# Kernel optimization log

Hardware: AMD Instinct MI355X
Metric: run time of the kernel (lower is better)

## Reference

```python
import jax, jax.numpy as jnp
import numpy as np

D_MODEL = 1024
NUM_HEADS = 16
THETA = 10000.0
NEG = -1000000.0  # masked_fill value used by the torch code


def _rope(x, token_positions, theta):
    # x: [B, H, S, d_head]; token_positions: [S] int
    d_k = x.shape[-1]
    half = d_k // 2
    j = jnp.arange(half, dtype=jnp.float32)
    inv_freq = theta ** (-(2.0 * j) / d_k)                      # [half]
    ang = token_positions.astype(jnp.float32)[:, None] * inv_freq  # [S, half]
    cos = jnp.cos(ang)
    sin = jnp.sin(ang)
    xp = x.reshape(x.shape[:-1] + (half, 2))  # adjacent pairs (pc, 2)
    x0, x1 = xp[..., 0], xp[..., 1]
    o0 = x0 * cos - x1 * sin
    o1 = x0 * sin + x1 * cos
    out = jnp.stack([o0, o1], axis=-1)
    return out.reshape(x.shape)


def setup_inputs() -> dict:
    key = jax.random.key(0)
    k0, k1, k2 = jax.random.split(key, 3)
    B, S, D = 2, 2048, D_MODEL
    std = (2.0 / (D + D)) ** 0.5
    X = jax.random.normal(k0, (B, S, D), dtype=jnp.float32)
    QKV_weights = jax.random.normal(k1, (3 * D, D), dtype=jnp.float32) * std
    O_weights = jax.random.normal(k2, (D, D), dtype=jnp.float32) * std
    token_positions = jnp.arange(S, dtype=jnp.int32)
    return {"X": X, "token_positions": token_positions,
            "QKV_weights": QKV_weights, "O_weights": O_weights}


def reference(X, token_positions, QKV_weights, O_weights):
    B, S, D = X.shape
    H = NUM_HEADS
    dh = D // H
    qkv = jnp.einsum('od,bsd->bso', QKV_weights, X)  # [B, S, 3D]
    Q, K, V = jnp.split(qkv, 3, axis=-1)

    def split_heads(t):
        return t.reshape(B, S, H, dh).transpose(0, 2, 1, 3)  # [B,H,S,dh]

    Q, K, V = split_heads(Q), split_heads(K), split_heads(V)
    Q = _rope(Q, token_positions, THETA)
    K = _rope(K, token_positions, THETA)

    scores = (jnp.einsum('bhqd,bhkd->bhqk', Q, K) / jnp.sqrt(jnp.float32(dh))).astype(jnp.float32)
    causal = jnp.tril(jnp.ones((S, S), dtype=bool))
    scores = jnp.where(causal, scores, NEG)
    probs = jax.nn.softmax(scores, axis=-1)
    attn = jnp.einsum('bhqk,bhkd->bhqd', probs, V.astype(jnp.float32)).astype(Q.dtype)
    attn = attn.transpose(0, 2, 1, 3).reshape(B, S, D)
    return jnp.einsum('od,bsd->bso', O_weights, attn)
```

## Files before the change

kernel.cpp:

```cpp
#include <hip/hip_runtime.h>
#include <math.h>

#define S_LEN 2048

using bf16x8  = __attribute__((ext_vector_type(8))) short;
using shortx4 = __attribute__((ext_vector_type(4))) short;
using f32x4   = __attribute__((ext_vector_type(4))) float;

static __device__ __forceinline__ short f2bf(float f) {
  unsigned u = __float_as_uint(f);
  u += 0x7fffu + ((u >> 16) & 1u);
  return (short)(u >> 16);
}
static __device__ __forceinline__ float bf2f(short s) {
  return __uint_as_float(((unsigned)(unsigned short)s) << 16);
}

#define GLD_LDS16(gptr, lptr)                                                  \
  __builtin_amdgcn_global_load_lds(                                            \
      (__attribute__((address_space(1))) void*)(gptr),                         \
      (__attribute__((address_space(3))) void*)(lptr), 16, 0, 0)

#define EXP2_SHIFT 20.0f

static __device__ __forceinline__ f32x4 exp2s4(f32x4 a) {
  return (f32x4){__builtin_amdgcn_exp2f(a[0] - EXP2_SHIFT),
                 __builtin_amdgcn_exp2f(a[1] - EXP2_SHIFT),
                 __builtin_amdgcn_exp2f(a[2] - EXP2_SHIFT),
                 __builtin_amdgcn_exp2f(a[3] - EXP2_SHIFT)};
}

__global__ __launch_bounds__(256) void init_kernel(const float* __restrict__ X,
                                                   const float* __restrict__ W1,
                                                   const float* __restrict__ W2,
                                                   const int* __restrict__ tok,
                                                   short* __restrict__ Xb,
                                                   short* __restrict__ W1b,
                                                   short* __restrict__ W2b,
                                                   float2* __restrict__ table) {
  if (blockIdx.x < 4096) {
    size_t idx = (size_t)(blockIdx.x * 256 + threadIdx.x) * 8;
    const float* src;
    short* dst;
    size_t off;
    if (idx < 4194304) { src = X; dst = Xb; off = idx; }
    else if (idx < 4194304 + 3145728) { src = W1; dst = W1b; off = idx - 4194304; }
    else { src = W2; dst = W2b; off = idx - (4194304 + 3145728); }
    float4 a = *(const float4*)(src + off);
    float4 b = *(const float4*)(src + off + 4);
    bf16x8 o = {f2bf(a.x), f2bf(a.y), f2bf(a.z), f2bf(a.w),
                f2bf(b.x), f2bf(b.y), f2bf(b.z), f2bf(b.w)};
    *(bf16x8*)(dst + off) = o;
  } else {
    int i = (blockIdx.x - 4096) * 256 + threadIdx.x;
    int s = i >> 5, j = i & 31;
    double pos = (double)tok[s];
    double ang = pos * pow(10000.0, -(double)j / 32.0);
    table[i] = make_float2((float)cos(ang), (float)sin(ang));
  }
}

template <int BM, typename OutT>
__global__ __launch_bounds__(256) void gemm_ll(const short* __restrict__ A,
                                               const short* __restrict__ B,
                                               OutT* __restrict__ C,
                                               int M, int N, int K) {
  constexpr int MI = BM / 32;
  constexpr int AI = BM / 64;
  __shared__ short As[BM * 32];
  __shared__ short Bs[128 * 32];
  const int tid  = threadIdx.x;
  const int lane = tid & 63;
  const int wv   = tid >> 6;
  const int wm   = (wv >> 1) * (BM / 2);
  const int wn   = (wv & 1) * 64;
  const int m16  = lane & 15;
  const int q4   = lane >> 4;
  const int rowBase = blockIdx.y * BM;
  const int colBase = blockIdx.x * 128;
  const int lrow = lane >> 2;
  const int lseg = lane & 3;

  f32x4 acc[MI][4];
#pragma unroll
  for (int i = 0; i < MI; ++i)
#pragma unroll
    for (int j = 0; j < 4; ++j) acc[i][j] = (f32x4){0.f, 0.f, 0.f, 0.f};

  const short* Agl = A + (size_t)rowBase * K;
  const short* Bgl = B + (size_t)colBase * K;

  for (int kk = 0; kk < K; kk += 32) {
#pragma unroll
    for (int i = 0; i < AI; ++i) {
      const int r0 = (wv * AI + i) * 16;
      GLD_LDS16(Agl + (size_t)(r0 + lrow) * K + kk + lseg * 8, &As[r0 * 32]);
    }
#pragma unroll
    for (int i = 0; i < 2; ++i) {
      const int r0 = (wv * 2 + i) * 16;
      GLD_LDS16(Bgl + (size_t)(r0 + lrow) * K + kk + lseg * 8, &Bs[r0 * 32]);
    }
    __syncthreads();

    bf16x8 af[MI], bfv[4];
#pragma unroll
    for (int mi = 0; mi < MI; ++mi)
      af[mi] = *(const bf16x8*)&As[(wm + mi * 16 + m16) * 32 + q4 * 8];
#pragma unroll
    for (int ni = 0; ni < 4; ++ni)
      bfv[ni] = *(const bf16x8*)&Bs[(wn + ni * 16 + m16) * 32 + q4 * 8];
#pragma unroll
    for (int mi = 0; mi < MI; ++mi)
#pragma unroll
      for (int ni = 0; ni < 4; ++ni)
        acc[mi][ni] = __builtin_amdgcn_mfma_f32_16x16x32_bf16(af[mi], bfv[ni], acc[mi][ni], 0, 0, 0);
    __syncthreads();
  }

#pragma unroll
  for (int mi = 0; mi < MI; ++mi)
#pragma unroll
    for (int ni = 0; ni < 4; ++ni) {
      const int rbase = rowBase + wm + mi * 16 + q4 * 4;
      const int cidx  = colBase + wn + ni * 16 + m16;
#pragma unroll
      for (int r = 0; r < 4; ++r) {
        float v = acc[mi][ni][r];
        if constexpr (sizeof(OutT) == 2)
          C[(size_t)(rbase + r) * N + cidx] = (OutT)f2bf(v);
        else
          C[(size_t)(rbase + r) * N + cidx] = (OutT)v;
      }
    }
}

__global__ __launch_bounds__(256) void prep_kernel(const short* __restrict__ qkvb,
                                                   const float2* __restrict__ table,
                                                   short* __restrict__ Qb,
                                                   short* __restrict__ Kb,
                                                   short* __restrict__ VT) {
  __shared__ __align__(16) short VtL[64 * 72];
  const int tid = threadIdx.x;
  const int st  = blockIdx.x, bh = blockIdx.y;
  const int b   = bh >> 4, h = bh & 15;
  const int r   = tid >> 2, seg = tid & 3;
  const int s   = st * 64 + r;
  const int pr  = (r & 15) * 4 + (r >> 4);
  const short* base = qkvb + (size_t)(b * S_LEN + s) * 3072 + h * 64 + seg * 16;
  const float QSCALE = 0.125f * 1.44269504f;

#pragma unroll
  for (int which = 0; which < 2; ++which) {
    const short* src = base + which * 1024;
    short in[16], ob[16];
    *(bf16x8*)&in[0] = ((const bf16x8*)src)[0];
    *(bf16x8*)&in[8] = ((const bf16x8*)src)[1];
#pragma unroll
    for (int p = 0; p < 8; ++p) {
      float x0 = bf2f(in[2 * p]), x1 = bf2f(in[2 * p + 1]);
      float2 cs = table[s * 32 + seg * 8 + p];
      float o0 = x0 * cs.x - x1 * cs.y;
      float o1 = x0 * cs.y + x1 * cs.x;
      if (which == 0) { o0 *= QSCALE; o1 *= QSCALE; }
      ob[2 * p]     = f2bf(o0);
      ob[2 * p + 1] = f2bf(o1);
    }
    short* dst = (which ? Kb : Qb) + ((size_t)bh * S_LEN + s) * 64 + seg * 16;
    ((bf16x8*)dst)[0] = *(bf16x8*)&ob[0];
    ((bf16x8*)dst)[1] = *(bf16x8*)&ob[8];
  }

  {
    const short* vsrc = base + 2048;
    short in[16];
    *(bf16x8*)&in[0] = ((const bf16x8*)vsrc)[0];
    *(bf16x8*)&in[8] = ((const bf16x8*)vsrc)[1];
#pragma unroll
    for (int d = 0; d < 16; ++d)
      VtL[(seg * 16 + d) * 72 + pr] = in[d];
  }
  __syncthreads();
  short* vdst = VT + ((size_t)bh * 64 + r) * S_LEN + st * 64 + seg * 16;
  ((bf16x8*)vdst)[0] = *(bf16x8*)&VtL[r * 72 + seg * 16];
  ((bf16x8*)vdst)[1] = *(bf16x8*)&VtL[r * 72 + seg * 16 + 8];
}

__global__ __launch_bounds__(256, 2) void attn_mfma(const short* __restrict__ Qb,
                                                    const short* __restrict__ Kb,
                                                    const short* __restrict__ VT,
                                                    short* __restrict__ attnb) {
  __shared__ __align__(16) short Ks[64 * 72];
  __shared__ __align__(16) short Vs[64 * 72];
  __shared__ __align__(16) short Ps[128 * 72];
  const int tid  = threadIdx.x;
  const int lane = tid & 63;
  const int w    = tid >> 6;
  const int m16  = lane & 15;
  const int quad = lane >> 4;
  const int bh   = blockIdx.x;
  const int jt   = 15 - blockIdx.y;
  const int b    = bh >> 4, h = bh & 15;
  const short* Qh = Qb + (size_t)bh * S_LEN * 64;
  const short* Kh = Kb + (size_t)bh * S_LEN * 64;
  const short* Vh = VT + (size_t)bh * 64 * S_LEN;

  const int srow = tid >> 3;
  const int seg  = tid & 7;

  const bf16x8 ones = {16256, 16256, 16256, 16256, 16256, 16256, 16256, 16256};

  const int q0 = jt * 128;
  const int ktiles = 2 * jt + 2;

  bf16x8 qf[2][2];
#pragma unroll
  for (int m = 0; m < 2; ++m)
#pragma unroll
    for (int ks = 0; ks < 2; ++ks)
      qf[m][ks] = *(const bf16x8*)(Qh + (size_t)(q0 + w * 32 + m * 16 + m16) * 64 + ks * 32 + quad * 8);

  f32x4 O[2][4], Lacc[2];
#pragma unroll
  for (int m = 0; m < 2; ++m) {
    Lacc[m] = (f32x4){0.f, 0.f, 0.f, 0.f};
#pragma unroll
    for (int c = 0; c < 4; ++c) O[m][c] = (f32x4){0.f, 0.f, 0.f, 0.f};
  }

  bf16x8 kst[2], vst[2];
#pragma unroll
  for (int i = 0; i < 2; ++i) {
    kst[i] = *(const bf16x8*)(Kh + (size_t)(i * 32 + srow) * 64 + seg * 8);
    vst[i] = *(const bf16x8*)(Vh + (size_t)(i * 32 + srow) * S_LEN + seg * 8);
  }

  for (int t = 0; t < ktiles; ++t) {
    {
#pragma unroll
      for (int i = 0; i < 2; ++i) {
        *(bf16x8*)&Ks[(i * 32 + srow) * 72 + seg * 8] = kst[i];
        *(bf16x8*)&Vs[(i * 32 + srow) * 72 + seg * 8] = vst[i];
      }
    }
    __syncthreads();

    if (t + 1 < ktiles) {
#pragma unroll
      for (int i = 0; i < 2; ++i) {
        kst[i] = *(const bf16x8*)(Kh + (size_t)((t + 1) * 64 + i * 32 + srow) * 64 + seg * 8);
        vst[i] = *(const bf16x8*)(Vh + (size_t)(i * 32 + srow) * S_LEN + (t + 1) * 64 + seg * 8);
      }
    }

    f32x4 sc[2][4];
#pragma unroll
    for (int m = 0; m < 2; ++m)
#pragma unroll
      for (int c = 0; c < 4; ++c) sc[m][c] = (f32x4){0.f, 0.f, 0.f, 0.f};
#pragma unroll
    for (int ks = 0; ks < 2; ++ks) {
#pragma unroll
      for (int c = 0; c < 4; ++c) {
        bf16x8 kf = *(const bf16x8*)&Ks[(c * 16 + m16) * 72 + ks * 32 + quad * 8];
#pragma unroll
        for (int m = 0; m < 2; ++m)
          sc[m][c] = __builtin_amdgcn_mfma_f32_16x16x32_bf16(qf[m][ks], kf, sc[m][c], 0, 0, 0);
      }
    }

    if (t >= ktiles - 2) {
#pragma unroll
      for (int m = 0; m < 2; ++m)
#pragma unroll
        for (int c = 0; c < 4; ++c) {
          const int kg = t * 64 + c * 16 + m16;
#pragma unroll
          for (int rr = 0; rr < 4; ++rr) {
            const int qg = q0 + w * 32 + m * 16 + quad * 4 + rr;
            if (kg > qg) sc[m][c][rr] = -1e30f;
          }
        }
    }

#pragma unroll
    for (int m = 0; m < 2; ++m) {
#pragma unroll
      for (int c = 0; c < 4; ++c) sc[m][c] = exp2s4(sc[m][c]);
#pragma unroll
      for (int rr = 0; rr < 4; ++rr) {
        shortx4 pk = {f2bf(sc[m][0][rr]), f2bf(sc[m][1][rr]),
                      f2bf(sc[m][2][rr]), f2bf(sc[m][3][rr])};
        *(shortx4*)&Ps[(w * 32 + m * 16 + quad * 4 + rr) * 72 + m16 * 4] = pk;
      }
    }
    __syncthreads();

#pragma unroll
    for (int ks = 0; ks < 2; ++ks) {
      bf16x8 pa[2];
#pragma unroll
      for (int m = 0; m < 2; ++m)
        pa[m] = *(const bf16x8*)&Ps[(w * 32 + m * 16 + m16) * 72 + ks * 32 + quad * 8];
#pragma unroll
      for (int c = 0; c < 4; ++c) {
        bf16x8 vb = *(const bf16x8*)&Vs[(c * 16 + m16) * 72 + ks * 32 + quad * 8];
#pragma unroll
        for (int m = 0; m < 2; ++m)
          O[m][c] = __builtin_amdgcn_mfma_f32_16x16x32_bf16(pa[m], vb, O[m][c], 0, 0, 0);
      }
#pragma unroll
      for (int m = 0; m < 2; ++m)
        Lacc[m] = __builtin_amdgcn_mfma_f32_16x16x32_bf16(pa[m], ones, Lacc[m], 0, 0, 0);
    }
    __syncthreads();
  }

#pragma unroll
  for (int m = 0; m < 2; ++m) {
    float inv[4];
#pragma unroll
    for (int rr = 0; rr < 4; ++rr) inv[rr] = __frcp_rn(Lacc[m][rr]);
#pragma unroll
    for (int c = 0; c < 4; ++c) {
      const int col = h * 64 + c * 16 + m16;
#pragma unroll
      for (int rr = 0; rr < 4; ++rr) {
        const int q = q0 + w * 32 + m * 16 + quad * 4 + rr;
        attnb[(size_t)(b * S_LEN + q) * 1024 + col] = f2bf(O[m][c][rr] * inv[rr]);
      }
    }
  }
}

extern "C" void kernel_launch(void* const* d_in, const int* in_sizes, int n_in,
                              void* d_out, int out_size, void* d_ws, size_t ws_size,
                              hipStream_t stream) {
  const float* X    = (const float*)d_in[0];
  const int*   tok  = (const int*)d_in[1];
  const float* Wqkv = (const float*)d_in[2];
  const float* Wo   = (const float*)d_in[3];
  float* out = (float*)d_out;

  char* w = (char*)d_ws;
  float2* table = (float2*)w;
  short*  qkvb  = (short*)(w + 524288);
  short*  Qb    = (short*)(w + 524288 + 25165824);
  short*  Kb    = Qb + 4194304;
  short*  VTt   = Kb + 4194304;
  short*  Xb    = VTt + 4194304;
  short*  Wqkvb = Xb + 4194304;
  short*  Wob   = Wqkvb + 3145728;
  short*  attnb = qkvb;

  hipLaunchKernelGGL(init_kernel, dim3(4352), dim3(256), 0, stream,
                     X, Wqkv, Wo, tok, Xb, Wqkvb, Wob, table);
  hipLaunchKernelGGL((gemm_ll<128, short>), dim3(24, 32), dim3(256), 0, stream,
                     Xb, Wqkvb, qkvb, 4096, 3072, 1024);
  hipLaunchKernelGGL(prep_kernel, dim3(32, 32), dim3(256), 0, stream,
                     qkvb, table, Qb, Kb, VTt);
  hipLaunchKernelGGL(attn_mfma, dim3(32, 16), dim3(256), 0, stream,
                     Qb, Kb, VTt, attnb);
  hipLaunchKernelGGL((gemm_ll<64, float>), dim3(8, 64), dim3(256), 0, stream,
                     attnb, Wob, out, 4096, 1024, 1024);
}
```

Measured before the change: 193.9 us.

## Compute transposed S^T so P stays in registers, dropping LDS round trip

```diff
diff --git a/kernel.cpp b/kernel.cpp
--- a/kernel.cpp
+++ b/kernel.cpp
@@ -28,6 +28,10 @@
                  __builtin_amdgcn_exp2f(a[1] - EXP2_SHIFT),
                  __builtin_amdgcn_exp2f(a[2] - EXP2_SHIFT),
                  __builtin_amdgcn_exp2f(a[3] - EXP2_SHIFT)};
+}
+
+static __device__ __forceinline__ int sigma64(int k) {
+  return (k & 0x20) | ((k & 0x0C) << 1) | ((k & 0x10) >> 2) | (k & 3);
 }
 
 __global__ __launch_bounds__(256) void init_kernel(const float* __restrict__ X,
@@ -146,7 +150,7 @@
   const int b   = bh >> 4, h = bh & 15;
   const int r   = tid >> 2, seg = tid & 3;
   const int s   = st * 64 + r;
-  const int pr  = (r & 15) * 4 + (r >> 4);
+  const int pr  = sigma64(r);
   const short* base = qkvb + (size_t)(b * S_LEN + s) * 3072 + h * 64 + seg * 16;
   const float QSCALE = 0.125f * 1.44269504f;
 
@@ -190,16 +194,17 @@
                                                     const short* __restrict__ Kb,
                                                     const short* __restrict__ VT,
                                                     short* __restrict__ attnb) {
-  __shared__ __align__(16) short Ks[64 * 72];
-  __shared__ __align__(16) short Vs[64 * 72];
-  __shared__ __align__(16) short Ps[128 * 72];
+  __shared__ __align__(16) short Smem[9216];
+  short* Ks = Smem;
+  short* Vs = Smem + 64 * 72;
   const int tid  = threadIdx.x;
   const int lane = tid & 63;
   const int w    = tid >> 6;
   const int m16  = lane & 15;
-  const int quad = lane >> 4;
+  const int q4   = lane >> 4;
   const int bh   = blockIdx.x;
-  const int jt   = 15 - blockIdx.y;
+  const int jtx  = blockIdx.y;
+  const int jt   = (jtx < 8) ? (15 - jtx) : (jtx - 8);
   const int b    = bh >> 4, h = bh & 15;
   const short* Qh = Qb + (size_t)bh * S_LEN * 64;
   const short* Kh = Kb + (size_t)bh * S_LEN * 64;
@@ -215,17 +220,17 @@
 
   bf16x8 qf[2][2];
 #pragma unroll
-  for (int m = 0; m < 2; ++m)
+  for (int n = 0; n < 2; ++n)
 #pragma unroll
     for (int ks = 0; ks < 2; ++ks)
-      qf[m][ks] = *(const bf16x8*)(Qh + (size_t)(q0 + w * 32 + m * 16 + m16) * 64 + ks * 32 + quad * 8);
+      qf[n][ks] = *(const bf16x8*)(Qh + (size_t)(q0 + w * 32 + n * 16 + m16) * 64 + ks * 32 + q4 * 8);
 
   f32x4 O[2][4], Lacc[2];
 #pragma unroll
-  for (int m = 0; m < 2; ++m) {
-    Lacc[m] = (f32x4){0.f, 0.f, 0.f, 0.f};
-#pragma unroll
-    for (int c = 0; c < 4; ++c) O[m][c] = (f32x4){0.f, 0.f, 0.f, 0.f};
+  for (int n = 0; n < 2; ++n) {
+    Lacc[n] = (f32x4){0.f, 0.f, 0.f, 0.f};
+#pragma unroll
+    for (int c = 0; c < 4; ++c) O[n][c] = (f32x4){0.f, 0.f, 0.f, 0.f};
   }
 
   bf16x8 kst[2], vst[2];
@@ -236,12 +241,10 @@
   }
 
   for (int t = 0; t < ktiles; ++t) {
-    {
-#pragma unroll
-      for (int i = 0; i < 2; ++i) {
-        *(bf16x8*)&Ks[(i * 32 + srow) * 72 + seg * 8] = kst[i];
-        *(bf16x8*)&Vs[(i * 32 + srow) * 72 + seg * 8] = vst[i];
-      }
+#pragma unroll
+    for (int i = 0; i < 2; ++i) {
+      *(bf16x8*)&Ks[(i * 32 + srow) * 72 + seg * 8] = kst[i];
+      *(bf16x8*)&Vs[(i * 32 + srow) * 72 + seg * 8] = vst[i];
     }
     __syncthreads();
 
@@ -255,81 +258,80 @@
 
     f32x4 sc[2][4];
 #pragma unroll
-    for (int m = 0; m < 2; ++m)
-#pragma unroll
-      for (int c = 0; c < 4; ++c) sc[m][c] = (f32x4){0.f, 0.f, 0.f, 0.f};
+    for (int n = 0; n < 2; ++n)
+#pragma unroll
+      for (int c = 0; c < 4; ++c) sc[n][c] = (f32x4){0.f, 0.f, 0.f, 0.f};
 #pragma unroll
     for (int ks = 0; ks < 2; ++ks) {
 #pragma unroll
       for (int c = 0; c < 4; ++c) {
-        bf16x8 kf = *(const bf16x8*)&Ks[(c * 16 + m16) * 72 + ks * 32 + quad * 8];
-#pragma unroll
-        for (int m = 0; m < 2; ++m)
-          sc[m][c] = __builtin_amdgcn_mfma_f32_16x16x32_bf16(qf[m][ks], kf, sc[m][c], 0, 0, 0);
+        bf16x8 kf = *(const bf16x8*)&Ks[(c * 16 + m16) * 72 + ks * 32 + q4 * 8];
+#pragma unroll
+        for (int n = 0; n < 2; ++n)
+          sc[n][c] = __builtin_amdgcn_mfma_f32_16x16x32_bf16(kf, qf[n][ks], sc[n][c], 0, 0, 0);
       }
     }
 
     if (t >= ktiles - 2) {
 #pragma unroll
-      for (int m = 0; m < 2; ++m)
+      for (int n = 0; n < 2; ++n)
 #pragma unroll
         for (int c = 0; c < 4; ++c) {
-          const int kg = t * 64 + c * 16 + m16;
+          const int qg = q0 + w * 32 + n * 16 + m16;
 #pragma unroll
           for (int rr = 0; rr < 4; ++rr) {
-            const int qg = q0 + w * 32 + m * 16 + quad * 4 + rr;
-            if (kg > qg) sc[m][c][rr] = -1e30f;
+            const int kg = t * 64 + c * 16 + q4 * 4 + rr;
+            if (kg > qg) sc[n][c][rr] = -1e30f;
           }
         }
     }
 
-#pragma unroll
-    for (int m = 0; m < 2; ++m) {
-#pragma unroll
-      for (int c = 0; c < 4; ++c) sc[m][c] = exp2s4(sc[m][c]);
-#pragma unroll
-      for (int rr = 0; rr < 4; ++rr) {
-        shortx4 pk = {f2bf(sc[m][0][rr]), f2bf(sc[m][1][rr]),
-                      f2bf(sc[m][2][rr]), f2bf(sc[m][3][rr])};
-        *(shortx4*)&Ps[(w * 32 + m * 16 + quad * 4 + rr) * 72 + m16 * 4] = pk;
+    bf16x8 pb[2][2];
+#pragma unroll
+    for (int n = 0; n < 2; ++n) {
+#pragma unroll
+      for (int c = 0; c < 4; ++c) sc[n][c] = exp2s4(sc[n][c]);
+      pb[n][0] = (bf16x8){f2bf(sc[n][0][0]), f2bf(sc[n][0][1]), f2bf(sc[n][0][2]), f2bf(sc[n][0][3]),
+                          f2bf(sc[n][1][0]), f2bf(sc[n][1][1]), f2bf(sc[n][1][2]), f2bf(sc[n][1][3])};
+      pb[n][1] = (bf16x8){f2bf(sc[n][2][0]), f2bf(sc[n][2][1]), f2bf(sc[n][2][2]), f2bf(sc[n][2][3]),
+                          f2bf(sc[n][3][0]), f2bf(sc[n][3][1]), f2bf(sc[n][3][2]), f2bf(sc[n][3][3])};
+    }
+
+#pragma unroll
+    for (int ch = 0; ch < 2; ++ch) {
+#pragma unroll
+      for (int c2 = 0; c2 < 4; ++c2) {
+        bf16x8 va = *(const bf16x8*)&Vs[(c2 * 16 + m16) * 72 + ch * 32 + q4 * 8];
+#pragma unroll
+        for (int n = 0; n < 2; ++n)
+          O[n][c2] = __builtin_amdgcn_mfma_f32_16x16x32_bf16(va, pb[n][ch], O[n][c2], 0, 0, 0);
       }
+#pragma unroll
+      for (int n = 0; n < 2; ++n)
+        Lacc[n] = __builtin_amdgcn_mfma_f32_16x16x32_bf16(ones, pb[n][ch], Lacc[n], 0, 0, 0);
     }
     __syncthreads();
-
-#pragma unroll
-    for (int ks = 0; ks < 2; ++ks) {
-      bf16x8 pa[2];
-#pragma unroll
-      for (int m = 0; m < 2; ++m)
-        pa[m] = *(const bf16x8*)&Ps[(w * 32 + m * 16 + m16) * 72 + ks * 32 + quad * 8];
-#pragma unroll
-      for (int c = 0; c < 4; ++c) {
-        bf16x8 vb = *(const bf16x8*)&Vs[(c * 16 + m16) * 72 + ks * 32 + quad * 8];
-#pragma unroll
-        for (int m = 0; m < 2; ++m)
-          O[m][c] = __builtin_amdgcn_mfma_f32_16x16x32_bf16(pa[m], vb, O[m][c], 0, 0, 0);
-      }
-#pragma unroll
-      for (int m = 0; m < 2; ++m)
-        Lacc[m] = __builtin_amdgcn_mfma_f32_16x16x32_bf16(pa[m], ones, Lacc[m], 0, 0, 0);
-    }
-    __syncthreads();
-  }
-
-#pragma unroll
-  for (int m = 0; m < 2; ++m) {
-    float inv[4];
-#pragma unroll
-    for (int rr = 0; rr < 4; ++rr) inv[rr] = __frcp_rn(Lacc[m][rr]);
-#pragma unroll
-    for (int c = 0; c < 4; ++c) {
-      const int col = h * 64 + c * 16 + m16;
-#pragma unroll
-      for (int rr = 0; rr < 4; ++rr) {
-        const int q = q0 + w * 32 + m * 16 + quad * 4 + rr;
-        attnb[(size_t)(b * S_LEN + q) * 1024 + col] = f2bf(O[m][c][rr] * inv[rr]);
-      }
-    }
+  }
+
+#pragma unroll
+  for (int n = 0; n < 2; ++n) {
+    const float inv = __frcp_rn(Lacc[n][0]);
+#pragma unroll
+    for (int c2 = 0; c2 < 4; ++c2) {
+      shortx4 ov = {f2bf(O[n][c2][0] * inv), f2bf(O[n][c2][1] * inv),
+                    f2bf(O[n][c2][2] * inv), f2bf(O[n][c2][3] * inv)};
+      *(shortx4*)&Smem[(w * 32 + n * 16 + m16) * 72 + c2 * 16 + q4 * 4] = ov;
+    }
+  }
+  __syncthreads();
+  {
+    const int row = tid >> 1, hf = tid & 1;
+    const short* src = &Smem[row * 72 + hf * 32];
+    short* dst = attnb + (size_t)(b * S_LEN + q0 + row) * 1024 + h * 64 + hf * 32;
+    ((bf16x8*)dst)[0] = ((const bf16x8*)src)[0];
+    ((bf16x8*)dst)[1] = ((const bf16x8*)src)[1];
+    ((bf16x8*)dst)[2] = ((const bf16x8*)src)[2];
+    ((bf16x8*)dst)[3] = ((const bf16x8*)src)[3];
   }
 }
 
```

New measurement: 184.7 us. 4.7% less time.
